# Performance work log

Hardware: AMD Instinct MI355X
Metric: run time of the kernel (lower is better)

The kernel has to match this reference:

```python
import jax, jax.numpy as jnp
import numpy as np

ALPHA = 0.2   # LeakyReLU negative slope
EPS = 1e-16   # guard for zero-degree row-sum (those rows are overwritten by x anyway)


def gat_layer(x, W, a, src, dst, n_nodes, concat):
    """One SpGraphAttentionLayer (eval mode, dropout disabled).
    edge_e = exp(-leakyrelu(a . [h_src || h_dst])); h' = spmm(e, h_dst) / rowsum(e).
    """
    h = x @ W                                   # [N, F]
    f = h.shape[-1]
    s_src = h @ a[:f]                           # [N]  a . h_src part
    s_dst = h @ a[f:]                           # [N]  a . h_dst part
    score = s_src[src] + s_dst[dst]             # [E]
    edge_e = jnp.exp(-jax.nn.leaky_relu(score, ALPHA))
    rowsum = jax.ops.segment_sum(edge_e, src, num_segments=n_nodes)          # [N]
    msg = jax.ops.segment_sum(edge_e[:, None] * h[dst], src, num_segments=n_nodes)  # [N, F]
    h_prime = msg / (rowsum[:, None] + EPS)
    return jax.nn.elu(h_prime) if concat else h_prime


def setup_inputs() -> dict:
    key = jax.random.key(0)
    ks = jax.random.split(key, 6)
    N, E = 100000, 3200000
    nfeat, nhid, nout, nheads = 128, 64, 128, 8
    x = jax.random.normal(ks[0], (N, nfeat), jnp.float32)
    edge_index = jax.random.randint(ks[1], (2, E), 0, N)
    W1 = jax.random.normal(ks[2], (nheads, nfeat, nhid), jnp.float32) * (1.0 / np.sqrt(nfeat))
    a1 = jax.random.normal(ks[3], (nheads, 2 * nhid), jnp.float32) * 0.1
    W2 = jax.random.normal(ks[4], (nheads * nhid, nout), jnp.float32) * (1.0 / np.sqrt(nheads * nhid))
    a2 = jax.random.normal(ks[5], (2 * nout,), jnp.float32) * 0.1
    return {"x": x, "edge_index": edge_index, "W1": W1, "a1": a1, "W2": W2, "a2": a2}


def reference(x, edge_index, W1, a1, W2, a2):
    N = x.shape[0]
    src, dst = edge_index[0], edge_index[1]
    # degree (== dense adj.sum(1)) for the zero-degree fallback h[flag] = x[flag]
    deg = jax.ops.segment_sum(jnp.ones(src.shape[0], jnp.float32), src, num_segments=N)
    # multi-head attention, concat=True (ELU inside each head), Python loop over fixed head count
    heads = [gat_layer(x, W1[i], a1[i], src, dst, N, True) for i in range(W1.shape[0])]
    x_ = jnp.concatenate(heads, axis=1)          # [N, nheads*nhid]
    h = gat_layer(x_, W2, a2, src, dst, N, False)  # [N, nout]
    h = jnp.where((deg == 0.0)[:, None], x, h)     # h[flag] = x[flag]
    return jax.nn.elu(h)
```

## Files before the change

kernel.cpp:

```cpp
#include <hip/hip_runtime.h>
#include <hip/hip_fp16.h>

#define NFEAT 128
#define NHID 64
#define NOUT 128
#define NHEADS 8
#define ALPHA_SLOPE 0.2f
#define EPS_DENOM 1e-16f

#define MAXNB 1024
#define BIN_EPB 12288
#define BIN_CAP 6144

typedef _Float16 f16;
typedef f16 f16x8 __attribute__((ext_vector_type(8)));
typedef float f32x4 __attribute__((ext_vector_type(4)));

static __device__ __forceinline__ float elu_f(float v) {
  return v > 0.f ? v : __expf(v) - 1.f;
}
static __device__ __forceinline__ float edge_w(float sc) {
  float lr = sc > 0.f ? sc : ALPHA_SLOPE * sc;
  return __expf(-lr);
}

__global__ void k_cvt_w(const float* __restrict__ W1, const float* __restrict__ W2,
                        const float* __restrict__ a1,
                        f16* __restrict__ w1t, f16* __restrict__ w2t,
                        f16* __restrict__ uv16) {
  int idx = blockIdx.x * 256 + threadIdx.x;
  if (idx < NHEADS * 128 * 64) {
    int h = idx >> 13, rem = idx & 8191, c = rem >> 7, k = rem & 127;
    w1t[idx] = (f16)W1[h * 8192 + k * 64 + c];
  } else if (idx < 2 * NHEADS * 128 * 64) {
    int j = idx - NHEADS * 128 * 64;
    int c = j >> 9, k = j & 511;
    w2t[j] = (f16)W2[k * 128 + c];
  } else {
    int id = idx - 2 * NHEADS * 128 * 64;
    if (id < 1024) {
      int h = id >> 7, k = id & 127;
      const float* wrow = W1 + h * 8192 + k * 64;
      const float* ah = a1 + h * 128;
      float u = 0.f, v = 0.f;
      for (int c = 0; c < 64; ++c) {
        float wv_ = wrow[c];
        u += wv_ * ah[c];
        v += wv_ * ah[64 + c];
      }
      uv16[h * 128 + k] = (f16)u;
      uv16[(8 + h) * 128 + k] = (f16)v;
    }
  }
}

__global__ __launch_bounds__(256) void k_prep_x(
    const float* __restrict__ x, const f16* __restrict__ uv16,
    f16* __restrict__ xh, float* __restrict__ ssrc8, f16* __restrict__ sdst8h, int N) {
  int wave = threadIdx.x >> 6, lane = threadIdx.x & 63;
  int c = lane & 15, g = lane >> 4;
  int row0 = blockIdx.x * 64 + wave * 16;
  f16x8 bf[4];
#pragma unroll
  for (int ks = 0; ks < 4; ++ks)
    bf[ks] = *(const f16x8*)(uv16 + c * 128 + ks * 32 + g * 8);
  int arow = row0 + c; if (arow > N - 1) arow = N - 1;
  const float* xp = x + (size_t)arow * 128 + g * 8;
  f16* xhp = xh + (size_t)arow * 128 + g * 8;
  f32x4 acc = (f32x4){0.f, 0.f, 0.f, 0.f};
#pragma unroll
  for (int ks = 0; ks < 4; ++ks) {
    float4 v0 = *(const float4*)(xp + ks * 32);
    float4 v1 = *(const float4*)(xp + ks * 32 + 4);
    f16x8 af;
    af[0] = (f16)v0.x; af[1] = (f16)v0.y; af[2] = (f16)v0.z; af[3] = (f16)v0.w;
    af[4] = (f16)v1.x; af[5] = (f16)v1.y; af[6] = (f16)v1.z; af[7] = (f16)v1.w;
    *(f16x8*)(xhp + ks * 32) = af;
    acc = __builtin_amdgcn_mfma_f32_16x16x32_f16(af, bf[ks], acc, 0, 0, 0);
  }
#pragma unroll
  for (int j = 0; j < 4; ++j) {
    int r = row0 + g * 4 + j;
    if (r < N) {
      if (c < 8) ssrc8[(size_t)r * 8 + c] = acc[j];
      else       sdst8h[(size_t)r * 8 + c - 8] = (f16)acc[j];
    }
  }
}

__global__ __launch_bounds__(256) void k_bhist(const int* __restrict__ src,
                                               int* __restrict__ bhist,
                                               int E, int NB, int shift) {
  __shared__ int h[MAXNB];
  int tid = threadIdx.x;
  for (int i = tid; i < NB; i += 256) h[i] = 0;
  __syncthreads();
  int base = blockIdx.x * BIN_EPB;
#pragma unroll 4
  for (int j = 0; j < BIN_EPB / 256; ++j) {
    int e = base + tid + j * 256;
    if (e < E) atomicAdd(&h[src[e] >> shift], 1);
  }
  __syncthreads();
  for (int i = tid; i < NB; i += 256)
    if (h[i]) atomicAdd(&bhist[i], h[i]);
}

__global__ __launch_bounds__(1024) void k_bscan(const int* __restrict__ bhist,
                                                int* __restrict__ bucket_base,
                                                int* __restrict__ bucket_cursor,
                                                int* __restrict__ rp,
                                                int NB, int N, int E) {
  __shared__ int sh[1024];
  int i = threadIdx.x;
  int v = (i < NB) ? bhist[i] : 0;
  sh[i] = v;
  __syncthreads();
  for (int off = 1; off < 1024; off <<= 1) {
    int add = (i >= off) ? sh[i - off] : 0;
    __syncthreads();
    sh[i] += add;
    __syncthreads();
  }
  if (i < NB) {
    int ex = sh[i] - v;
    bucket_base[i] = ex;
    bucket_cursor[i] = ex;
  }
  if (i == 0) {
    bucket_base[NB] = E;
    rp[N] = E;
  }
}

__global__ __launch_bounds__(256) void k_binA(const int* __restrict__ src,
                                              const int* __restrict__ dst,
                                              int* __restrict__ bucket_cursor,
                                              int2* __restrict__ staging,
                                              int E, int NB, int shift) {
  __shared__ int h[MAXNB];
  int tid = threadIdx.x;
  for (int i = tid; i < NB; i += 256) h[i] = 0;
  __syncthreads();
  int base = blockIdx.x * BIN_EPB;
#pragma unroll 4
  for (int j = 0; j < BIN_EPB / 256; ++j) {
    int e = base + tid + j * 256;
    if (e < E) atomicAdd(&h[src[e] >> shift], 1);
  }
  __syncthreads();
  for (int i = tid; i < NB; i += 256)
    if (h[i]) h[i] = atomicAdd(&bucket_cursor[i], h[i]);
  __syncthreads();
#pragma unroll 4
  for (int j = 0; j < BIN_EPB / 256; ++j) {
    int e = base + tid + j * 256;
    if (e < E) {
      int s = src[e];
      int slot = atomicAdd(&h[s >> shift], 1);
      staging[slot] = make_int2(s, dst[e]);
    }
  }
}

__global__ __launch_bounds__(256) void k_binB(const int2* __restrict__ staging,
                                              const int* __restrict__ bucket_base,
                                              int* __restrict__ rp,
                                              int* __restrict__ edge_dst,
                                              int N, int shift) {
  __shared__ int2 buf[BIN_CAP];
  __shared__ int rcnt[256], rsc[256];
  int tid = threadIdx.x;
  int b = blockIdx.x;
  int lo = bucket_base[b], hi = bucket_base[b + 1];
  int S = hi - lo;
  if (S > BIN_CAP) S = BIN_CAP;
  int R = 1 << shift;
  int rmask = R - 1;
  for (int i = tid; i < S; i += 256) buf[i] = staging[lo + i];
  if (tid < R) rcnt[tid] = 0;
  __syncthreads();
  for (int i = tid; i < S; i += 256) atomicAdd(&rcnt[buf[i].x & rmask], 1);
  __syncthreads();
  if (tid < R) rsc[tid] = rcnt[tid];
  __syncthreads();
  for (int off = 1; off < 256; off <<= 1) {
    int add = (tid >= off && tid < R) ? rsc[tid - off] : 0;
    __syncthreads();
    if (tid < R) rsc[tid] += add;
    __syncthreads();
  }
  int row0 = b << shift;
  if (tid < R) {
    int ex = rsc[tid] - rcnt[tid];
    rcnt[tid] = ex;
    if (row0 + tid < N) rp[row0 + tid] = lo + ex;
  }
  __syncthreads();
  for (int i = tid; i < S; i += 256) {
    int r = buf[i].x & rmask;
    int k = atomicAdd(&rcnt[r], 1);
    edge_dst[lo + k] = buf[i].y;
  }
}

__global__ __launch_bounds__(256) void k_aggx(
    const int* __restrict__ rp, const int* __restrict__ edge_dst,
    const f16* __restrict__ xh, const float* __restrict__ ssrc8,
    const f16* __restrict__ sdst8h, f16* __restrict__ msgx, int c0, int c1) {
  __shared__ __half wbuf[4][64][8];
  int wv4 = threadIdx.x >> 6;
  int lane = threadIdx.x & 63;
  int node = c0 + blockIdx.x * 4 + wv4;
  if (node >= c1) return;
  int e0 = rp[node], e1 = rp[node + 1];
  int hi = lane >> 5, li = lane & 31;
  float4 sA = *(const float4*)(ssrc8 + (size_t)node * 8);
  float4 sB = *(const float4*)(ssrc8 + (size_t)node * 8 + 4);
  float acc[8][4];
#pragma unroll
  for (int h = 0; h < 8; ++h)
#pragma unroll
    for (int cc = 0; cc < 4; ++cc) acc[h][cc] = 0.f;
  float rs[8];
#pragma unroll
  for (int h = 0; h < 8; ++h) rs[h] = 0.f;
  __half* wb = &wbuf[wv4][0][0];

  for (int base = e0; base < e1; base += 64) {
    int cnt = e1 - base; if (cnt > 64) cnt = 64;
    int d = 0;
    float w0 = 0.f, w1 = 0.f, w2 = 0.f, w3 = 0.f, w4 = 0.f, w5 = 0.f, w6 = 0.f, w7 = 0.f;
    if (lane < cnt) {
      d = edge_dst[base + lane];
      f16x8 dv = *(const f16x8*)(sdst8h + (size_t)d * 8);
      w0 = edge_w(sA.x + (float)dv[0]); w1 = edge_w(sA.y + (float)dv[1]);
      w2 = edge_w(sA.z + (float)dv[2]); w3 = edge_w(sA.w + (float)dv[3]);
      w4 = edge_w(sB.x + (float)dv[4]); w5 = edge_w(sB.y + (float)dv[5]);
      w6 = edge_w(sB.z + (float)dv[6]); w7 = edge_w(sB.w + (float)dv[7]);
      rs[0] += w0; rs[1] += w1; rs[2] += w2; rs[3] += w3;
      rs[4] += w4; rs[5] += w5; rs[6] += w6; rs[7] += w7;
    }
    float4 pk;
    ((__half2*)&pk)[0] = __float22half2_rn(make_float2(w0, w1));
    ((__half2*)&pk)[1] = __float22half2_rn(make_float2(w2, w3));
    ((__half2*)&pk)[2] = __float22half2_rn(make_float2(w4, w5));
    ((__half2*)&pk)[3] = __float22half2_rn(make_float2(w6, w7));
    *(float4*)(wb + lane * 8) = pk;
    __threadfence_block();

    int jj = 0;
    for (; jj + 2 <= cnt; jj += 2) {
      int e = jj + hi;
      int de = __shfl(d, e);
      float4 wk = *(const float4*)(wb + e * 8);
      float2 wA = __half22float2(((__half2*)&wk)[0]);
      float2 wB = __half22float2(((__half2*)&wk)[1]);
      float2 wC = __half22float2(((__half2*)&wk)[2]);
      float2 wD = __half22float2(((__half2*)&wk)[3]);
      float2 xraw = *(const float2*)(xh + (size_t)de * 128 + li * 4);
      float2 x01 = __half22float2(((__half2*)&xraw)[0]);
      float2 x23 = __half22float2(((__half2*)&xraw)[1]);
      acc[0][0] += wA.x * x01.x; acc[0][1] += wA.x * x01.y; acc[0][2] += wA.x * x23.x; acc[0][3] += wA.x * x23.y;
      acc[1][0] += wA.y * x01.x; acc[1][1] += wA.y * x01.y; acc[1][2] += wA.y * x23.x; acc[1][3] += wA.y * x23.y;
      acc[2][0] += wB.x * x01.x; acc[2][1] += wB.x * x01.y; acc[2][2] += wB.x * x23.x; acc[2][3] += wB.x * x23.y;
      acc[3][0] += wB.y * x01.x; acc[3][1] += wB.y * x01.y; acc[3][2] += wB.y * x23.x; acc[3][3] += wB.y * x23.y;
      acc[4][0] += wC.x * x01.x; acc[4][1] += wC.x * x01.y; acc[4][2] += wC.x * x23.x; acc[4][3] += wC.x * x23.y;
      acc[5][0] += wC.y * x01.x; acc[5][1] += wC.y * x01.y; acc[5][2] += wC.y * x23.x; acc[5][3] += wC.y * x23.y;
      acc[6][0] += wD.x * x01.x; acc[6][1] += wD.x * x01.y; acc[6][2] += wD.x * x23.x; acc[6][3] += wD.x * x23.y;
      acc[7][0] += wD.y * x01.x; acc[7][1] += wD.y * x01.y; acc[7][2] += wD.y * x23.x; acc[7][3] += wD.y * x23.y;
    }
    if (jj < cnt) {
      int de = __shfl(d, jj);
      float4 wk = *(const float4*)(wb + jj * 8);
      if (hi == 0) {
        float2 wA = __half22float2(((__half2*)&wk)[0]);
        float2 wB = __half22float2(((__half2*)&wk)[1]);
        float2 wC = __half22float2(((__half2*)&wk)[2]);
        float2 wD = __half22float2(((__half2*)&wk)[3]);
        float2 xraw = *(const float2*)(xh + (size_t)de * 128 + li * 4);
        float2 x01 = __half22float2(((__half2*)&xraw)[0]);
        float2 x23 = __half22float2(((__half2*)&xraw)[1]);
        acc[0][0] += wA.x * x01.x; acc[0][1] += wA.x * x01.y; acc[0][2] += wA.x * x23.x; acc[0][3] += wA.x * x23.y;
        acc[1][0] += wA.y * x01.x; acc[1][1] += wA.y * x01.y; acc[1][2] += wA.y * x23.x; acc[1][3] += wA.y * x23.y;
        acc[2][0] += wB.x * x01.x; acc[2][1] += wB.x * x01.y; acc[2][2] += wB.x * x23.x; acc[2][3] += wB.x * x23.y;
        acc[3][0] += wB.y * x01.x; acc[3][1] += wB.y * x01.y; acc[3][2] += wB.y * x23.x; acc[3][3] += wB.y * x23.y;
        acc[4][0] += wC.x * x01.x; acc[4][1] += wC.x * x01.y; acc[4][2] += wC.x * x23.x; acc[4][3] += wC.x * x23.y;
        acc[5][0] += wC.y * x01.x; acc[5][1] += wC.y * x01.y; acc[5][2] += wC.y * x23.x; acc[5][3] += wC.y * x23.y;
        acc[6][0] += wD.x * x01.x; acc[6][1] += wD.x * x01.y; acc[6][2] += wD.x * x23.x; acc[6][3] += wD.x * x23.y;
        acc[7][0] += wD.y * x01.x; acc[7][1] += wD.y * x01.y; acc[7][2] += wD.y * x23.x; acc[7][3] += wD.y * x23.y;
      }
    }
  }

#pragma unroll
  for (int h = 0; h < 8; ++h)
#pragma unroll
    for (int cc = 0; cc < 4; ++cc) acc[h][cc] += __shfl_xor(acc[h][cc], 32);
#pragma unroll
  for (int off = 32; off > 0; off >>= 1)
#pragma unroll
    for (int h = 0; h < 8; ++h) rs[h] += __shfl_xor(rs[h], off);

  if (hi == 0) {
    f16* mp = msgx + (size_t)(node - c0) * 1024 + li * 4;
#pragma unroll
    for (int h = 0; h < 8; ++h) {
      float inv = 1.f / (rs[h] + EPS_DENOM);
      float2 st;
      ((__half2*)&st)[0] = __float22half2_rn(make_float2(acc[h][0] * inv, acc[h][1] * inv));
      ((__half2*)&st)[1] = __float22half2_rn(make_float2(acc[h][2] * inv, acc[h][3] * inv));
      *(float2*)(mp + h * 128) = st;
    }
  }
}

__global__ __launch_bounds__(256) void k_fusedgemm(
    const f16* __restrict__ msgx, const f16* __restrict__ w1t,
    const f16* __restrict__ w2t, const float* __restrict__ a2,
    f16* __restrict__ h2h, float* __restrict__ s2src, float* __restrict__ s2dst,
    int c0, int c1) {
  __shared__ f16 hl[4][32][68];
  int wave = threadIdx.x >> 6, lane = threadIdx.x & 63;
  int c = lane & 15, g = lane >> 4;
  int row0 = c0 + blockIdx.x * 128 + wave * 32;
  int ar0 = row0 + c;      if (ar0 > c1 - 1) ar0 = c1 - 1;
  int ar1 = row0 + 16 + c; if (ar1 > c1 - 1) ar1 = c1 - 1;

  f32x4 acc2[2][8];
#pragma unroll
  for (int jg = 0; jg < 2; ++jg)
#pragma unroll
    for (int t = 0; t < 8; ++t) acc2[jg][t] = (f32x4){0.f, 0.f, 0.f, 0.f};

#pragma unroll
  for (int h = 0; h < 8; ++h) {
    const f16* ap0 = msgx + ((size_t)(ar0 - c0) * 8 + h) * 128 + g * 8;
    const f16* ap1 = msgx + ((size_t)(ar1 - c0) * 8 + h) * 128 + g * 8;
    const f16* bp = w1t + (size_t)h * 8192;
    f32x4 acc[2][4];
#pragma unroll
    for (int jg = 0; jg < 2; ++jg)
#pragma unroll
      for (int t = 0; t < 4; ++t) acc[jg][t] = (f32x4){0.f, 0.f, 0.f, 0.f};
#pragma unroll
    for (int ks = 0; ks < 4; ++ks) {
      f16x8 af0 = *(const f16x8*)(ap0 + ks * 32);
      f16x8 af1 = *(const f16x8*)(ap1 + ks * 32);
#pragma unroll
      for (int t = 0; t < 4; ++t) {
        f16x8 bf = *(const f16x8*)(bp + (t * 16 + c) * 128 + ks * 32 + g * 8);
        acc[0][t] = __builtin_amdgcn_mfma_f32_16x16x32_f16(af0, bf, acc[0][t], 0, 0, 0);
        acc[1][t] = __builtin_amdgcn_mfma_f32_16x16x32_f16(af1, bf, acc[1][t], 0, 0, 0);
      }
    }
#pragma unroll
    for (int jg = 0; jg < 2; ++jg)
#pragma unroll
      for (int j = 0; j < 4; ++j)
#pragma unroll
        for (int t = 0; t < 4; ++t)
          hl[wave][jg * 16 + g * 4 + j][t * 16 + c] = (f16)elu_f(acc[jg][t][j]);

#pragma unroll
    for (int ks2 = 0; ks2 < 2; ++ks2) {
      f16x8 af0 = *(const f16x8*)&hl[wave][c][ks2 * 32 + g * 8];
      f16x8 af1 = *(const f16x8*)&hl[wave][16 + c][ks2 * 32 + g * 8];
#pragma unroll
      for (int t = 0; t < 8; ++t) {
        f16x8 bf = *(const f16x8*)(w2t + (size_t)(t * 16 + c) * 512 + h * 64 + ks2 * 32 + g * 8);
        acc2[0][t] = __builtin_amdgcn_mfma_f32_16x16x32_f16(af0, bf, acc2[0][t], 0, 0, 0);
        acc2[1][t] = __builtin_amdgcn_mfma_f32_16x16x32_f16(af1, bf, acc2[1][t], 0, 0, 0);
      }
    }
  }

  float av0[8], av1[8];
#pragma unroll
  for (int t = 0; t < 8; ++t) {
    av0[t] = a2[t * 16 + c];
    av1[t] = a2[128 + t * 16 + c];
  }
#pragma unroll
  for (int jg = 0; jg < 2; ++jg)
#pragma unroll
    for (int j = 0; j < 4; ++j) {
      int r = row0 + jg * 16 + g * 4 + j;
      float s0 = 0.f, s1 = 0.f;
#pragma unroll
      for (int t = 0; t < 8; ++t) {
        float v = acc2[jg][t][j];
        if (r < c1) h2h[(size_t)r * 128 + t * 16 + c] = (f16)v;
        s0 += v * av0[t];
        s1 += v * av1[t];
      }
      s0 += __shfl_xor(s0, 1); s0 += __shfl_xor(s0, 2);
      s0 += __shfl_xor(s0, 4); s0 += __shfl_xor(s0, 8);
      s1 += __shfl_xor(s1, 1); s1 += __shfl_xor(s1, 2);
      s1 += __shfl_xor(s1, 4); s1 += __shfl_xor(s1, 8);
      if (c == 0 && r < c1) { s2src[r] = s0; s2dst[r] = s1; }
    }
}

__global__ void k_agg2(const int* __restrict__ rp, const int* __restrict__ edge_dst,
                       const __half* __restrict__ h2h, const float* __restrict__ ssrc,
                       const float* __restrict__ sdst, const float* __restrict__ x,
                       float* __restrict__ out, int N) {
  int wv = (blockIdx.x * blockDim.x + threadIdx.x) >> 6;
  int lane = threadIdx.x & 63;
  if (wv >= N) return;
  int e0 = rp[wv], e1 = rp[wv + 1];
  if (e0 == e1) {
    float2 xv = *(const float2*)(x + (size_t)wv * 128 + 2 * lane);
    *(float2*)(out + (size_t)wv * 128 + 2 * lane) = make_float2(elu_f(xv.x), elu_f(xv.y));
    return;
  }
  float ss = ssrc[wv];
  int hi = lane >> 5;
  int colB = (lane & 31) << 2;
  float a0 = 0.f, a1 = 0.f, a2v = 0.f, a3 = 0.f, rsumL = 0.f;
  for (int base = e0; base < e1; base += 64) {
    int cnt = e1 - base; if (cnt > 64) cnt = 64;
    int d = 0; float w = 0.f;
    if (lane < cnt) {
      d = edge_dst[base + lane];
      w = edge_w(ss + sdst[d]);
    }
    rsumL += w;
    int jj = 0;
#pragma unroll 4
    for (; jj + 2 <= cnt; jj += 2) {
      int sel = jj + hi;
      int dj = __shfl(d, sel);
      float wj = __shfl(w, sel);
      float2 raw = *(const float2*)(h2h + ((size_t)dj << 7) + colB);
      float2 f01 = __half22float2(*(const __half2*)&raw.x);
      float2 f23 = __half22float2(*(const __half2*)&raw.y);
      a0 += wj * f01.x; a1 += wj * f01.y; a2v += wj * f23.x; a3 += wj * f23.y;
    }
    if (jj < cnt) {
      int dj = __shfl(d, jj);
      float wj = __shfl(w, jj);
      if (hi == 0) {
        float2 raw = *(const float2*)(h2h + ((size_t)dj << 7) + colB);
        float2 f01 = __half22float2(*(const __half2*)&raw.x);
        float2 f23 = __half22float2(*(const __half2*)&raw.y);
        a0 += wj * f01.x; a1 += wj * f01.y; a2v += wj * f23.x; a3 += wj * f23.y;
      }
    }
  }
  a0 += __shfl_xor(a0, 32); a1 += __shfl_xor(a1, 32);
  a2v += __shfl_xor(a2v, 32); a3 += __shfl_xor(a3, 32);
  float rsum = rsumL;
#pragma unroll
  for (int off = 32; off > 0; off >>= 1) rsum += __shfl_xor(rsum, off);
  float inv = 1.f / (rsum + EPS_DENOM);
  if (hi == 0) {
    *(float4*)(out + (size_t)wv * 128 + colB) =
        make_float4(elu_f(a0 * inv), elu_f(a1 * inv), elu_f(a2v * inv), elu_f(a3 * inv));
  }
}

extern "C" void kernel_launch(void* const* d_in, const int* in_sizes, int n_in,
                              void* d_out, int out_size, void* d_ws, size_t ws_size,
                              hipStream_t stream) {
  (void)n_in; (void)out_size;
  const float* x  = (const float*)d_in[0];
  const int*   ei = (const int*)d_in[1];
  const float* W1 = (const float*)d_in[2];
  const float* a1 = (const float*)d_in[3];
  const float* W2 = (const float*)d_in[4];
  const float* a2 = (const float*)d_in[5];
  float* out = (float*)d_out;
  const int N = in_sizes[0] / NFEAT;
  const int E = in_sizes[1] / 2;
  const int* src  = ei;
  const int* dstv = ei + E;

  int shift = 7;
  while ((((N - 1) >> shift) + 1) > MAXNB) ++shift;
  const int NB = ((N - 1) >> shift) + 1;

  int nc = 1;
  for (;;) {
    int cN = (N + nc - 1) / nc;
    size_t sz[15] = {
      (size_t)E * 8 > (size_t)cN * 2048 ? (size_t)E * 8 : (size_t)cN * 2048,
      (size_t)N * 256,
      (size_t)N * 256,
      (size_t)E * 4,
      (size_t)N * 32,
      (size_t)N * 16,
      (size_t)N * 4, (size_t)N * 4,
      (size_t)(N + 1) * 4,
      (size_t)(NB + 1) * 4, (size_t)(NB + 1) * 4, (size_t)(NB + 1) * 4,
      (size_t)NHEADS * 64 * 128 * 2,
      (size_t)128 * 512 * 2,
      (size_t)16 * 128 * 2
    };
    size_t need = 0;
    for (int i = 0; i < 15; ++i) need += (sz[i] + 255) & ~(size_t)255;
    need += 4096;
    if (need <= ws_size || nc >= 32) break;
    nc <<= 1;
  }
  const int chunkN = (N + nc - 1) / nc;

  char* wp = (char*)d_ws;
  size_t off = 0;
  auto mk = [&](size_t bytes) -> void* {
    void* p = wp + off;
    off += (bytes + 255) & ~(size_t)255;
    return p;
  };
  size_t szR0 = (size_t)E * 8;
  if ((size_t)chunkN * 2048 > szR0) szR0 = (size_t)chunkN * 2048;
  f16*  msgx     = (f16*)mk(szR0);
  int2* staging  = (int2*)msgx;
  f16*  h2h      = (f16*)mk((size_t)N * 128 * 2);
  f16*  xh       = (f16*)mk((size_t)N * 128 * 2);
  int*  edge_dst = (int*)mk((size_t)E * 4);
  float* ssrc8   = (float*)mk((size_t)N * 8 * 4);
  f16*  sdst8h   = (f16*)mk((size_t)N * 8 * 2);
  float* s2src   = (float*)mk((size_t)N * 4);
  float* s2dst   = (float*)mk((size_t)N * 4);
  int*  rp       = (int*)mk((size_t)(N + 1) * 4);
  int*  bhist    = (int*)mk((size_t)(NB + 1) * 4);
  int*  bbase    = (int*)mk((size_t)(NB + 1) * 4);
  int*  bcur     = (int*)mk((size_t)(NB + 1) * 4);
  f16*  w1t      = (f16*)mk((size_t)NHEADS * 64 * 128 * 2);
  f16*  w2t      = (f16*)mk((size_t)128 * 512 * 2);
  f16*  uv16     = (f16*)mk((size_t)16 * 128 * 2);

  k_cvt_w<<<516, 256, 0, stream>>>(W1, W2, a1, w1t, w2t, uv16);
  k_prep_x<<<(N + 63) / 64, 256, 0, stream>>>(x, uv16, xh, ssrc8, sdst8h, N);

  (void)hipMemsetAsync(bhist, 0, (size_t)NB * 4, stream);
  int binBlocks = (E + BIN_EPB - 1) / BIN_EPB;
  k_bhist<<<binBlocks, 256, 0, stream>>>(src, bhist, E, NB, shift);
  k_bscan<<<1, 1024, 0, stream>>>(bhist, bbase, bcur, rp, NB, N, E);
  k_binA<<<binBlocks, 256, 0, stream>>>(src, dstv, bcur, staging, E, NB, shift);
  k_binB<<<NB, 256, 0, stream>>>(staging, bbase, rp, edge_dst, N, shift);

  for (int ch = 0; ch < nc; ++ch) {
    int c0 = ch * chunkN;
    if (c0 >= N) break;
    int c1 = c0 + chunkN; if (c1 > N) c1 = N;
    int cn = c1 - c0;
    k_aggx<<<(cn + 3) / 4, 256, 0, stream>>>(rp, edge_dst, xh, ssrc8, sdst8h, msgx, c0, c1);
    k_fusedgemm<<<(cn + 127) / 128, 256, 0, stream>>>(msgx, w1t, w2t, a2, h2h,
                                                      s2src, s2dst, c0, c1);
  }

  int wb = (N + 3) / 4;
  k_agg2<<<wb, 256, 0, stream>>>(rp, edge_dst, (const __half*)h2h, s2src, s2dst, x, out, N);
}
```

Before: 698.1 us.

## Use packed fp16 dot2 with transposed edge-weight tile in layer-1 aggregation

Restructures the first-layer attention aggregation so each lane owns two feature columns across all 64 lanes, instead of splitting the wave into two halves of 32 lanes with four columns each. Edge weights are stored transposed in LDS as [head][edge]. Pairs of neighbour rows are interleaved with byte permutes, so the v_dot2 fp16 instruction can accumulate two edges per op. This is meant to cut VALU work and the cross-half reduction. In exchange, each gather load per edge is narrower, and products are formed in fp16 inputs with fp32 accumulation.

```diff
diff --git a/kernel.cpp b/kernel.cpp
--- a/kernel.cpp
+++ b/kernel.cpp
@@ -13,6 +13,7 @@
 #define BIN_CAP 6144
 
 typedef _Float16 f16;
+typedef f16 f16x2 __attribute__((ext_vector_type(2)));
 typedef f16 f16x8 __attribute__((ext_vector_type(8)));
 typedef float f32x4 __attribute__((ext_vector_type(4)));
 
@@ -22,6 +23,16 @@
 static __device__ __forceinline__ float edge_w(float sc) {
   float lr = sc > 0.f ? sc : ALPHA_SLOPE * sc;
   return __expf(-lr);
+}
+static __device__ __forceinline__ f16x2 u2h(unsigned int u) {
+  union { unsigned int u; f16x2 h; } c; c.u = u; return c.h;
+}
+static __device__ __forceinline__ float dot2f(f16x2 a, f16x2 b, float c) {
+#if __has_builtin(__builtin_amdgcn_fdot2)
+  return __builtin_amdgcn_fdot2(a, b, c, false);
+#else
+  return c + (float)a[0] * (float)b[0] + (float)a[1] * (float)b[1];
+#endif
 }
 
 __global__ void k_cvt_w(const float* __restrict__ W1, const float* __restrict__ W2,
@@ -208,24 +219,22 @@
     const int* __restrict__ rp, const int* __restrict__ edge_dst,
     const f16* __restrict__ xh, const float* __restrict__ ssrc8,
     const f16* __restrict__ sdst8h, f16* __restrict__ msgx, int c0, int c1) {
-  __shared__ __half wbuf[4][64][8];
-  int wv4 = threadIdx.x >> 6;
+  __shared__ __half wT[4][8][72];
+  int wave = threadIdx.x >> 6;
   int lane = threadIdx.x & 63;
-  int node = c0 + blockIdx.x * 4 + wv4;
+  int node = c0 + blockIdx.x * 4 + wave;
   if (node >= c1) return;
   int e0 = rp[node], e1 = rp[node + 1];
-  int hi = lane >> 5, li = lane & 31;
+  int col2 = lane * 2;
   float4 sA = *(const float4*)(ssrc8 + (size_t)node * 8);
   float4 sB = *(const float4*)(ssrc8 + (size_t)node * 8 + 4);
-  float acc[8][4];
-#pragma unroll
-  for (int h = 0; h < 8; ++h)
-#pragma unroll
-    for (int cc = 0; cc < 4; ++cc) acc[h][cc] = 0.f;
+  float acc[8][2];
+#pragma unroll
+  for (int h = 0; h < 8; ++h) { acc[h][0] = 0.f; acc[h][1] = 0.f; }
   float rs[8];
 #pragma unroll
   for (int h = 0; h < 8; ++h) rs[h] = 0.f;
-  __half* wb = &wbuf[wv4][0][0];
+  __half* wb = &wT[wave][0][0];
 
   for (int base = e0; base < e1; base += 64) {
     int cnt = e1 - base; if (cnt > 64) cnt = 64;
@@ -241,77 +250,63 @@
       rs[0] += w0; rs[1] += w1; rs[2] += w2; rs[3] += w3;
       rs[4] += w4; rs[5] += w5; rs[6] += w6; rs[7] += w7;
     }
-    float4 pk;
-    ((__half2*)&pk)[0] = __float22half2_rn(make_float2(w0, w1));
-    ((__half2*)&pk)[1] = __float22half2_rn(make_float2(w2, w3));
-    ((__half2*)&pk)[2] = __float22half2_rn(make_float2(w4, w5));
-    ((__half2*)&pk)[3] = __float22half2_rn(make_float2(w6, w7));
-    *(float4*)(wb + lane * 8) = pk;
+    wb[0 * 72 + lane] = __float2half(w0);
+    wb[1 * 72 + lane] = __float2half(w1);
+    wb[2 * 72 + lane] = __float2half(w2);
+    wb[3 * 72 + lane] = __float2half(w3);
+    wb[4 * 72 + lane] = __float2half(w4);
+    wb[5 * 72 + lane] = __float2half(w5);
+    wb[6 * 72 + lane] = __float2half(w6);
+    wb[7 * 72 + lane] = __float2half(w7);
     __threadfence_block();
 
     int jj = 0;
-    for (; jj + 2 <= cnt; jj += 2) {
-      int e = jj + hi;
-      int de = __shfl(d, e);
-      float4 wk = *(const float4*)(wb + e * 8);
-      float2 wA = __half22float2(((__half2*)&wk)[0]);
-      float2 wB = __half22float2(((__half2*)&wk)[1]);
-      float2 wC = __half22float2(((__half2*)&wk)[2]);
-      float2 wD = __half22float2(((__half2*)&wk)[3]);
-      float2 xraw = *(const float2*)(xh + (size_t)de * 128 + li * 4);
-      float2 x01 = __half22float2(((__half2*)&xraw)[0]);
-      float2 x23 = __half22float2(((__half2*)&xraw)[1]);
-      acc[0][0] += wA.x * x01.x; acc[0][1] += wA.x * x01.y; acc[0][2] += wA.x * x23.x; acc[0][3] += wA.x * x23.y;
-      acc[1][0] += wA.y * x01.x; acc[1][1] += wA.y * x01.y; acc[1][2] += wA.y * x23.x; acc[1][3] += wA.y * x23.y;
-      acc[2][0] += wB.x * x01.x; acc[2][1] += wB.x * x01.y; acc[2][2] += wB.x * x23.x; acc[2][3] += wB.x * x23.y;
-      acc[3][0] += wB.y * x01.x; acc[3][1] += wB.y * x01.y; acc[3][2] += wB.y * x23.x; acc[3][3] += wB.y * x23.y;
-      acc[4][0] += wC.x * x01.x; acc[4][1] += wC.x * x01.y; acc[4][2] += wC.x * x23.x; acc[4][3] += wC.x * x23.y;
-      acc[5][0] += wC.y * x01.x; acc[5][1] += wC.y * x01.y; acc[5][2] += wC.y * x23.x; acc[5][3] += wC.y * x23.y;
-      acc[6][0] += wD.x * x01.x; acc[6][1] += wD.x * x01.y; acc[6][2] += wD.x * x23.x; acc[6][3] += wD.x * x23.y;
-      acc[7][0] += wD.y * x01.x; acc[7][1] += wD.y * x01.y; acc[7][2] += wD.y * x23.x; acc[7][3] += wD.y * x23.y;
-    }
-    if (jj < cnt) {
-      int de = __shfl(d, jj);
-      float4 wk = *(const float4*)(wb + jj * 8);
-      if (hi == 0) {
-        float2 wA = __half22float2(((__half2*)&wk)[0]);
-        float2 wB = __half22float2(((__half2*)&wk)[1]);
-        float2 wC = __half22float2(((__half2*)&wk)[2]);
-        float2 wD = __half22float2(((__half2*)&wk)[3]);
-        float2 xraw = *(const float2*)(xh + (size_t)de * 128 + li * 4);
-        float2 x01 = __half22float2(((__half2*)&xraw)[0]);
-        float2 x23 = __half22float2(((__half2*)&xraw)[1]);
-        acc[0][0] += wA.x * x01.x; acc[0][1] += wA.x * x01.y; acc[0][2] += wA.x * x23.x; acc[0][3] += wA.x * x23.y;
-        acc[1][0] += wA.y * x01.x; acc[1][1] += wA.y * x01.y; acc[1][2] += wA.y * x23.x; acc[1][3] += wA.y * x23.y;
-        acc[2][0] += wB.x * x01.x; acc[2][1] += wB.x * x01.y; acc[2][2] += wB.x * x23.x; acc[2][3] += wB.x * x23.y;
-        acc[3][0] += wB.y * x01.x; acc[3][1] += wB.y * x01.y; acc[3][2] += wB.y * x23.x; acc[3][3] += wB.y * x23.y;
-        acc[4][0] += wC.x * x01.x; acc[4][1] += wC.x * x01.y; acc[4][2] += wC.x * x23.x; acc[4][3] += wC.x * x23.y;
-        acc[5][0] += wC.y * x01.x; acc[5][1] += wC.y * x01.y; acc[5][2] += wC.y * x23.x; acc[5][3] += wC.y * x23.y;
-        acc[6][0] += wD.x * x01.x; acc[6][1] += wD.x * x01.y; acc[6][2] += wD.x * x23.x; acc[6][3] += wD.x * x23.y;
-        acc[7][0] += wD.y * x01.x; acc[7][1] += wD.y * x01.y; acc[7][2] += wD.y * x23.x; acc[7][3] += wD.y * x23.y;
-      }
-    }
-  }
-
-#pragma unroll
-  for (int h = 0; h < 8; ++h)
-#pragma unroll
-    for (int cc = 0; cc < 4; ++cc) acc[h][cc] += __shfl_xor(acc[h][cc], 32);
+    for (; jj + 4 <= cnt; jj += 4) {
+      int d0 = __shfl(d, jj),     d1 = __shfl(d, jj + 1);
+      int d2 = __shfl(d, jj + 2), d3 = __shfl(d, jj + 3);
+      unsigned int ua = *(const unsigned int*)(xh + (size_t)d0 * 128 + col2);
+      unsigned int ub = *(const unsigned int*)(xh + (size_t)d1 * 128 + col2);
+      unsigned int uc = *(const unsigned int*)(xh + (size_t)d2 * 128 + col2);
+      unsigned int ud = *(const unsigned int*)(xh + (size_t)d3 * 128 + col2);
+      f16x2 XA0 = u2h(__builtin_amdgcn_perm(ub, ua, 0x05040100u));
+      f16x2 XA1 = u2h(__builtin_amdgcn_perm(ub, ua, 0x07060302u));
+      f16x2 XB0 = u2h(__builtin_amdgcn_perm(ud, uc, 0x05040100u));
+      f16x2 XB1 = u2h(__builtin_amdgcn_perm(ud, uc, 0x07060302u));
+#pragma unroll
+      for (int h = 0; h < 8; ++h) {
+        uint2 wq = *(const uint2*)(wb + h * 72 + jj);
+        f16x2 WA = u2h(wq.x), WB = u2h(wq.y);
+        acc[h][0] = dot2f(WA, XA0, acc[h][0]);
+        acc[h][0] = dot2f(WB, XB0, acc[h][0]);
+        acc[h][1] = dot2f(WA, XA1, acc[h][1]);
+        acc[h][1] = dot2f(WB, XB1, acc[h][1]);
+      }
+    }
+    for (; jj < cnt; ++jj) {
+      int dj = __shfl(d, jj);
+      unsigned int u = *(const unsigned int*)(xh + (size_t)dj * 128 + col2);
+      f16x2 xv = u2h(u);
+      float x0 = (float)xv[0], x1 = (float)xv[1];
+#pragma unroll
+      for (int h = 0; h < 8; ++h) {
+        float wh = __half2float(wb[h * 72 + jj]);
+        acc[h][0] += wh * x0;
+        acc[h][1] += wh * x1;
+      }
+    }
+  }
+
 #pragma unroll
   for (int off = 32; off > 0; off >>= 1)
 #pragma unroll
     for (int h = 0; h < 8; ++h) rs[h] += __shfl_xor(rs[h], off);
 
-  if (hi == 0) {
-    f16* mp = msgx + (size_t)(node - c0) * 1024 + li * 4;
-#pragma unroll
-    for (int h = 0; h < 8; ++h) {
-      float inv = 1.f / (rs[h] + EPS_DENOM);
-      float2 st;
-      ((__half2*)&st)[0] = __float22half2_rn(make_float2(acc[h][0] * inv, acc[h][1] * inv));
-      ((__half2*)&st)[1] = __float22half2_rn(make_float2(acc[h][2] * inv, acc[h][3] * inv));
-      *(float2*)(mp + h * 128) = st;
-    }
+  f16* mp = msgx + (size_t)(node - c0) * 1024 + col2;
+#pragma unroll
+  for (int h = 0; h < 8; ++h) {
+    float inv = 1.f / (rs[h] + EPS_DENOM);
+    __half2 st = __float22half2_rn(make_float2(acc[h][0] * inv, acc[h][1] * inv));
+    *(__half2*)(mp + h * 128) = st;
   }
 }
 
```

Result: faster. 629.8 us (-9.8%).
